# Kernel optimization log

Measured on AMD Instinct MI355X. Metric: run time of the kernel, lower is better.

Reference implementation:

```python
import jax, jax.numpy as jnp
import numpy as np

SIZE = 32  # voxel grid resolution (build_image default)
BIG = 1e9


def voxelize(points, vals, mask, size=SIZE):
    """Faithful dense re-expression of build_image's fractional box-overlap
    rasterization. points [P,3], vals [P], mask [P] -> volume [size,size,size].
    Each point is a cube of side grid_step in normalized coords; its value is
    splatted with separable fractional overlap onto the size^3 grid."""
    pm = jnp.where(mask[:, None], points, BIG)
    mins = jnp.min(pm, axis=0)
    maxs = jnp.max(jnp.where(mask[:, None], points, -BIG), axis=0)
    ranges = maxs - mins
    max_range = jnp.max(ranges) + 1.0
    gs = 1.0 / max_range                      # grid_step
    v = (points - mins - ranges / 2 - 0.5) * gs + 0.5   # [P,3] normalized cube mins
    ns = 1.0 / size                           # new_step
    lo = jnp.arange(size, dtype=points.dtype) * ns       # [S] cell lower edges
    # separable overlap fraction per axis: [P,3,S]
    ov = jnp.clip(jnp.minimum(v[:, :, None] + gs, lo + ns)
                  - jnp.maximum(v[:, :, None], lo), 0.0) / gs
    w = vals * mask.astype(vals.dtype)
    return jnp.einsum('p,pi,pj,pk->ijk', w, ov[:, 0], ov[:, 1], ov[:, 2])


def conv_block(x, W, b, stride):
    y = jax.lax.conv_general_dilated(
        x, W, (stride,) * 3, 'SAME',
        dimension_numbers=('NCDHW', 'OIDHW', 'NCDHW'))
    return jax.nn.relu(y + b[None, :, None, None, None])


def encoder(vox, W1, b1, W2, b2, W3, b3, Wfc, bfc):
    x = vox[:, None]                          # [E,1,32,32,32]
    x = conv_block(x, W1, b1, 2)              # [E,16,16,16,16]
    x = conv_block(x, W2, b2, 2)              # [E,32,8,8,8]
    x = conv_block(x, W3, b3, 2)              # [E,64,4,4,4]
    pooled = x.mean(axis=(2, 3, 4))           # [E,64]
    return pooled @ Wfc + bfc


def setup_inputs() -> dict:
    key = jax.random.key(0)
    ks = jax.random.split(key, 10)
    N, C, P, E = 32768, 256, 128, 1024
    data = jax.random.normal(ks[0], (N, 5), dtype=jnp.float32)
    clusts = jax.random.randint(ks[1], (C, P), 0, N, dtype=jnp.int32)
    clust_mask = jnp.ones((C, P), dtype=bool)
    edge_index = jax.random.randint(ks[2], (2, E), 0, C, dtype=jnp.int64)
    s = 0.1
    W1 = jax.random.normal(ks[3], (16, 1, 3, 3, 3), jnp.float32) * s
    b1 = jnp.zeros((16,), jnp.float32)
    W2 = jax.random.normal(ks[4], (32, 16, 3, 3, 3), jnp.float32) * s
    b2 = jnp.zeros((32,), jnp.float32)
    W3 = jax.random.normal(ks[5], (64, 32, 3, 3, 3), jnp.float32) * s
    b3 = jnp.zeros((64,), jnp.float32)
    Wfc = jax.random.normal(ks[6], (64, 64), jnp.float32) * s
    bfc = jnp.zeros((64,), jnp.float32)
    return {"data": data, "clusts": clusts, "clust_mask": clust_mask,
            "edge_index": edge_index, "W1": W1, "b1": b1, "W2": W2, "b2": b2,
            "W3": W3, "b3": b3, "Wfc": Wfc, "bfc": bfc}


def reference(data, clusts, clust_mask, edge_index, W1, b1, W2, b2, W3, b3, Wfc, bfc):
    # original detaches data before voxelization (numpy round-trip)
    d = jax.lax.stop_gradient(data)

    def edge_vox(cid):
        idx = clusts[cid]                     # [P]
        pts = d[idx, :3]
        vals = d[idx, 4]
        return voxelize(pts, vals, clust_mask[cid])

    ei, ej = edge_index[0], edge_index[1]
    # both clusters of an edge share the same sparse batch id i -> duplicate
    # coordinates sum, i.e. the two independently-normalized images add up
    vox = jax.vmap(edge_vox)(ei) + jax.vmap(edge_vox)(ej)   # [E,32,32,32]
    return encoder(vox, W1, b1, W2, b2, W3, b3, Wfc, bfc)   # [E,64]
```

## Files before the change

kernel.cpp:

```cpp
#include <hip/hip_runtime.h>

#define PPC 128

__device__ __forceinline__ float ovlap(float v, float gs, float inv_gs, int i) {
  const float ns = 0.03125f;
  float lo = (float)i * ns;
  float o  = fminf(v + gs, lo + ns) - fmaxf(v, lo);
  return fmaxf(o, 0.0f) * inv_gs;
}

__global__ __launch_bounds__(256) void k_vox_conv1(
    const float* __restrict__ data,
    const int*   __restrict__ clusts,
    const unsigned char* __restrict__ maskb,
    const float* __restrict__ W1,
    float* __restrict__ y1)
{
  __shared__ float vox[32768];
  __shared__ float rmn[PPC * 3];
  __shared__ float rmx[PPC * 3];
  const int c = blockIdx.x;
  const int t = threadIdx.x;

  for (int i = t; i < 32768; i += 256) vox[i] = 0.f;

  const bool m32 = (maskb[1] == 0);

  if (t < PPC) {
    int idx = clusts[c * PPC + t];
    const float* dp = data + idx * 5;
    bool m = m32 ? (((const int*)maskb)[c * PPC + t] != 0)
                 : (maskb[c * PPC + t] != 0);
#pragma unroll
    for (int d = 0; d < 3; ++d) {
      float p = dp[d];
      rmn[t * 3 + d] = m ? p : 1e9f;
      rmx[t * 3 + d] = m ? p : -1e9f;
    }
  }
  __syncthreads();
  for (int off = 64; off >= 1; off >>= 1) {
    if (t < off) {
#pragma unroll
      for (int d = 0; d < 3; ++d) {
        rmn[t * 3 + d] = fminf(rmn[t * 3 + d], rmn[(t + off) * 3 + d]);
        rmx[t * 3 + d] = fmaxf(rmx[t * 3 + d], rmx[(t + off) * 3 + d]);
      }
    }
    __syncthreads();
  }
  const float mn0 = rmn[0], mn1 = rmn[1], mn2 = rmn[2];
  const float rg0 = rmx[0] - mn0, rg1 = rmx[1] - mn1, rg2 = rmx[2] - mn2;
  const float mr = fmaxf(rg0, fmaxf(rg1, rg2)) + 1.0f;
  const float gs = 1.0f / mr;
  const float inv_gs = 1.0f / gs;

  {
    const int p = t >> 1, h = t & 1;
    int idx = clusts[c * PPC + p];
    const float* dp = data + idx * 5;
    bool m = m32 ? (((const int*)maskb)[c * PPC + p] != 0)
                 : (maskb[c * PPC + p] != 0);
    float w = m ? dp[4] : 0.f;
    if (w != 0.f) {
      float v0 = (dp[0] - mn0 - rg0 * 0.5f - 0.5f) * gs + 0.5f;
      float v1 = (dp[1] - mn1 - rg1 * 0.5f - 0.5f) * gs + 0.5f;
      float v2 = (dp[2] - mn2 - rg2 * 0.5f - 0.5f) * gs + 0.5f;
      int i0 = max(0, (int)floorf(v0 * 32.f) - 1), i1 = min(31, (int)floorf((v0 + gs) * 32.f) + 1);
      int j0 = max(0, (int)floorf(v1 * 32.f) - 1), j1 = min(31, (int)floorf((v1 + gs) * 32.f) + 1);
      int k0 = max(0, (int)floorf(v2 * 32.f) - 1), k1 = min(31, (int)floorf((v2 + gs) * 32.f) + 1);
      for (int i = i0 + h; i <= i1; i += 2) {
        float oi = ovlap(v0, gs, inv_gs, i);
        if (oi <= 0.f) continue;
        float wi = w * oi;
        for (int j = j0; j <= j1; ++j) {
          float oj = ovlap(v1, gs, inv_gs, j);
          if (oj <= 0.f) continue;
          float wij = wi * oj;
          for (int k = k0; k <= k1; ++k) {
            float ok = ovlap(v2, gs, inv_gs, k);
            if (ok > 0.f) atomicAdd(&vox[(i << 10) + (j << 5) + k], wij * ok);
          }
        }
      }
    }
  }
  __syncthreads();

  for (int si = 0; si < 16; ++si) {
    int s = t + (si << 8);
    int oz = s >> 8, oy = (s >> 4) & 15, ox = s & 15;
    float xv[27];
#pragma unroll
    for (int td = 0; td < 3; ++td)
#pragma unroll
      for (int th = 0; th < 3; ++th)
#pragma unroll
        for (int tw = 0; tw < 3; ++tw) {
          int z = 2 * oz + td, y = 2 * oy + th, x = 2 * ox + tw;
          bool okb = (z < 32) & (y < 32) & (x < 32);
          xv[(td * 3 + th) * 3 + tw] = okb ? vox[(z << 10) + (y << 5) + x] : 0.f;
        }
#pragma unroll
    for (int oc = 0; oc < 16; ++oc) {
      float a = 0.f;
#pragma unroll
      for (int tp = 0; tp < 27; ++tp) a = fmaf(W1[oc * 27 + tp], xv[tp], a);
      y1[(((c << 4) + oc) << 12) + s] = a;
    }
  }
}

#define S1 4913
__global__ __launch_bounds__(256) void k_edge(
    const void*  __restrict__ eidx_raw,
    const float* __restrict__ y1,
    const float* __restrict__ b1,
    const float* __restrict__ W2,
    const float* __restrict__ b2,
    const float* __restrict__ W3,
    const float* __restrict__ b3,
    const float* __restrict__ Wfc,
    const float* __restrict__ bfc,
    float* __restrict__ out,
    int E)
{
  __shared__ float smem[2 * S1 + 64];
  float* pooled = smem + 2 * S1;
  const int e = blockIdx.x;
  const int t = threadIdx.x;

  const int* e32 = (const int*)eidx_raw;
  const long long* e64 = (const long long*)eidx_raw;
  const bool is64 = (e32[1] == 0) & (e32[3] == 0) & (e32[5] == 0) & (e32[7] == 0);
  const int ca = is64 ? (int)e64[e] : e32[e];
  const int cb = is64 ? (int)e64[E + e] : e32[E + e];
  const float* Ap = y1 + (size_t)ca * 65536;
  const float* Bp = y1 + (size_t)cb * 65536;

  float acc2[2][32];
#pragma unroll
  for (int h = 0; h < 2; ++h)
#pragma unroll
    for (int o = 0; o < 32; ++o) acc2[h][o] = 0.f;

  const int oz0 = t >> 6, oy0 = (t >> 3) & 7, ox0 = t & 7;
  const int xl = t & 15;
  const int stw = (t >> 4) * 17 + (xl >> 1) + (xl & 1) * 9;

  for (int i = t; i < 2 * S1; i += 256) smem[i] = 0.f;

  {
    const float bb = b1[0];
#pragma unroll 4
    for (int z = 0; z < 16; ++z)
      smem[stw + z * 289] = fmaxf(Ap[(z << 8) + t] + Bp[(z << 8) + t] + bb, 0.f);
  }
  __syncthreads();

#pragma unroll 2
  for (int ic = 0; ic < 16; ++ic) {
    if (ic < 15) {
      const int icn = ic + 1;
      const float* Aic = Ap + (icn << 12);
      const float* Bic = Bp + (icn << 12);
      const float bb = b1[icn];
      const int wb = (icn & 1) * S1 + stw;
#pragma unroll 4
      for (int z = 0; z < 16; ++z)
        smem[wb + z * 289] = fmaxf(Aic[(z << 8) + t] + Bic[(z << 8) + t] + bb, 0.f);
    }
    {
      const int rb = (ic & 1) * S1 + oz0 * 578 + oy0 * 34;
      float xv0[27], xv1[27];
#pragma unroll
      for (int td = 0; td < 3; ++td)
#pragma unroll
        for (int th = 0; th < 3; ++th) {
          const int b0 = rb + td * 289 + th * 17;
          const int tpb = (td * 3 + th) * 3;
          xv0[tpb + 0] = smem[b0 + ox0];
          xv0[tpb + 1] = smem[b0 + 9 + ox0];
          xv0[tpb + 2] = smem[b0 + ox0 + 1];
          xv1[tpb + 0] = smem[b0 + 2312 + ox0];
          xv1[tpb + 1] = smem[b0 + 2312 + 9 + ox0];
          xv1[tpb + 2] = smem[b0 + 2312 + ox0 + 1];
        }
      const float* wrow = W2 + ic * 27;
#pragma unroll
      for (int oc = 0; oc < 32; ++oc) {
#pragma unroll
        for (int tp = 0; tp < 27; ++tp) {
          const float w = wrow[oc * 432 + tp];
          acc2[0][oc] = fmaf(w, xv0[tp], acc2[0][oc]);
          acc2[1][oc] = fmaf(w, xv1[tp], acc2[1][oc]);
        }
      }
    }
    __syncthreads();
  }

  float acc3[16];
#pragma unroll
  for (int o = 0; o < 16; ++o) acc3[o] = 0.f;
  const int l = t & 63, wid = t >> 6;
  const int OZ = l >> 4, OY = (l >> 2) & 3, OX = l & 3;
  const int rb3 = OZ * 162 + OY * 18;
  const int cox = (ox0 >> 1) + (ox0 & 1) * 5;

#pragma unroll
  for (int q = 0; q < 4; ++q) {
    for (int i = t; i < 5832; i += 256) smem[i] = 0.f;
    __syncthreads();
#pragma unroll
    for (int h = 0; h < 2; ++h)
#pragma unroll
      for (int o = 0; o < 8; ++o) {
        const int oc = (q << 3) + o;
        smem[o * 729 + (oz0 + (h << 2)) * 81 + oy0 * 9 + cox] =
            fmaxf(acc2[h][oc] + b2[oc], 0.f);
      }
    __syncthreads();
#pragma unroll 1
    for (int icl = 0; icl < 8; ++icl) {
      const int ic3 = (q << 3) + icl;
      float xv[27];
#pragma unroll
      for (int td = 0; td < 3; ++td)
#pragma unroll
        for (int th = 0; th < 3; ++th) {
          const int bb = icl * 729 + rb3 + td * 81 + th * 9;
          const int tpb = (td * 3 + th) * 3;
          xv[tpb + 0] = smem[bb + OX];
          xv[tpb + 1] = smem[bb + 5 + OX];
          xv[tpb + 2] = smem[bb + OX + 1];
        }
#pragma unroll
      for (int o = 0; o < 16; ++o) {
        const int oc = (wid << 4) + o;
        const float* wr = W3 + (oc * 32 + ic3) * 27;
#pragma unroll
        for (int tp = 0; tp < 27; ++tp) acc3[o] = fmaf(wr[tp], xv[tp], acc3[o]);
      }
    }
    __syncthreads();
  }

#pragma unroll
  for (int o = 0; o < 16; ++o) {
    float r = fmaxf(acc3[o] + b3[(wid << 4) + o], 0.f);
    r += __shfl_xor(r, 1);
    r += __shfl_xor(r, 2);
    r += __shfl_xor(r, 4);
    r += __shfl_xor(r, 8);
    r += __shfl_xor(r, 16);
    r += __shfl_xor(r, 32);
    if (l == 0) pooled[(wid << 4) + o] = r * 0.015625f;
  }
  __syncthreads();
  if (t < 64) {
    float a = bfc[t];
#pragma unroll 8
    for (int k = 0; k < 64; ++k) a = fmaf(pooled[k], Wfc[(k << 6) + t], a);
    out[e * 64 + t] = a;
  }
}

extern "C" void kernel_launch(void* const* d_in, const int* in_sizes, int n_in,
                              void* d_out, int out_size, void* d_ws, size_t ws_size,
                              hipStream_t stream) {
  const float* data = (const float*)d_in[0];
  const int*   clusts = (const int*)d_in[1];
  const unsigned char* maskb = (const unsigned char*)d_in[2];
  const void*  eidx = d_in[3];
  const float* W1 = (const float*)d_in[4];
  const float* b1 = (const float*)d_in[5];
  const float* W2 = (const float*)d_in[6];
  const float* b2 = (const float*)d_in[7];
  const float* W3 = (const float*)d_in[8];
  const float* b3 = (const float*)d_in[9];
  const float* Wfc = (const float*)d_in[10];
  const float* bfc = (const float*)d_in[11];

  const int C = in_sizes[1] / PPC;
  const int E = in_sizes[3] / 2;

  float* y1 = (float*)d_ws;

  k_vox_conv1<<<C, 256, 0, stream>>>(data, clusts, maskb, W1, y1);
  k_edge<<<E, 256, 0, stream>>>(eidx, y1, b1, W2, b2, W3, b3, Wfc, bfc,
                                (float*)d_out, E);
}
```

Baseline: 930.4 us.

## Vectorize staging loads and interleave prefetch with conv2/conv3 tap loops

Staging of the conv1 output (A+B+bias, relu) into shared memory now uses float4 global loads with a remapped store pattern. The loads for the next input channel are split into two halves and issued between groups of the conv2 tap loop, so global latency overlaps with FMAs. The conv2 and conv3 inner loops are restructured to load three taps at a time instead of holding 27-element register arrays, which is meant to reduce register pressure. The conv3 shared buffer is zeroed once rather than per quarter, relying on the halo staying zero across quarters. The risks are the extra synchronisation added at the start and possible changes to scheduling and register allocation.

```diff
diff --git a/kernel.cpp b/kernel.cpp
--- a/kernel.cpp
+++ b/kernel.cpp
@@ -145,60 +145,116 @@
     for (int o = 0; o < 32; ++o) acc2[h][o] = 0.f;
 
   const int oz0 = t >> 6, oy0 = (t >> 3) & 7, ox0 = t & 7;
-  const int xl = t & 15;
-  const int stw = (t >> 4) * 17 + (xl >> 1) + (xl & 1) * 9;
+  const int zl = t >> 6, lane63 = t & 63, xq = t & 3;
+  const int stwb = ((t >> 2) & 15) * 17 + 2 * xq;
 
   for (int i = t; i < 2 * S1; i += 256) smem[i] = 0.f;
+  __syncthreads();
 
   {
+    const float4* A4 = (const float4*)Ap;
+    const float4* B4 = (const float4*)Bp;
     const float bb = b1[0];
-#pragma unroll 4
-    for (int z = 0; z < 16; ++z)
-      smem[stw + z * 289] = fmaxf(Ap[(z << 8) + t] + Bp[(z << 8) + t] + bb, 0.f);
+#pragma unroll
+    for (int b = 0; b < 4; ++b) {
+      const int z = (b << 2) + zl;
+      float4 av = A4[(z << 6) + lane63];
+      float4 bv = B4[(z << 6) + lane63];
+      const int w = z * 289 + stwb;
+      smem[w]      = fmaxf(av.x + bv.x + bb, 0.f);
+      smem[w + 9]  = fmaxf(av.y + bv.y + bb, 0.f);
+      smem[w + 1]  = fmaxf(av.z + bv.z + bb, 0.f);
+      smem[w + 10] = fmaxf(av.w + bv.w + bb, 0.f);
+    }
   }
   __syncthreads();
 
 #pragma unroll 2
   for (int ic = 0; ic < 16; ++ic) {
-    if (ic < 15) {
-      const int icn = ic + 1;
-      const float* Aic = Ap + (icn << 12);
-      const float* Bic = Bp + (icn << 12);
-      const float bb = b1[icn];
-      const int wb = (icn & 1) * S1 + stw;
-#pragma unroll 4
-      for (int z = 0; z < 16; ++z)
-        smem[wb + z * 289] = fmaxf(Aic[(z << 8) + t] + Bic[(z << 8) + t] + bb, 0.f);
-    }
-    {
-      const int rb = (ic & 1) * S1 + oz0 * 578 + oy0 * 34;
-      float xv0[27], xv1[27];
-#pragma unroll
-      for (int td = 0; td < 3; ++td)
-#pragma unroll
-        for (int th = 0; th < 3; ++th) {
-          const int b0 = rb + td * 289 + th * 17;
-          const int tpb = (td * 3 + th) * 3;
-          xv0[tpb + 0] = smem[b0 + ox0];
-          xv0[tpb + 1] = smem[b0 + 9 + ox0];
-          xv0[tpb + 2] = smem[b0 + ox0 + 1];
-          xv1[tpb + 0] = smem[b0 + 2312 + ox0];
-          xv1[tpb + 1] = smem[b0 + 2312 + 9 + ox0];
-          xv1[tpb + 2] = smem[b0 + 2312 + ox0 + 1];
-        }
-      const float* wrow = W2 + ic * 27;
+    const int rb = (ic & 1) * S1 + oz0 * 578 + oy0 * 34;
+    const float* wrow = W2 + ic * 27;
+    const bool st = (ic < 15);
+    const float4* An4 = (const float4*)(Ap + ((ic + 1) << 12));
+    const float4* Bn4 = (const float4*)(Bp + ((ic + 1) << 12));
+    const float bb = st ? b1[ic + 1] : 0.f;
+    const int wb = ((ic + 1) & 1) * S1;
+
+    float4 a0, a1, c0, c1;
+    if (st) {
+      a0 = An4[(zl << 6) + lane63];        c0 = Bn4[(zl << 6) + lane63];
+      a1 = An4[((4 + zl) << 6) + lane63];  c1 = Bn4[((4 + zl) << 6) + lane63];
+    }
+#pragma unroll
+    for (int g = 0; g < 4; ++g) {
+      const int td = g / 3, th = g % 3;
+      const int b0 = rb + td * 289 + th * 17;
+      float t00 = smem[b0 + ox0], t01 = smem[b0 + 9 + ox0], t02 = smem[b0 + ox0 + 1];
+      float t10 = smem[b0 + 2312 + ox0], t11 = smem[b0 + 2312 + 9 + ox0], t12 = smem[b0 + 2312 + ox0 + 1];
+      const int tp = g * 3;
 #pragma unroll
       for (int oc = 0; oc < 32; ++oc) {
-#pragma unroll
-        for (int tp = 0; tp < 27; ++tp) {
-          const float w = wrow[oc * 432 + tp];
-          acc2[0][oc] = fmaf(w, xv0[tp], acc2[0][oc]);
-          acc2[1][oc] = fmaf(w, xv1[tp], acc2[1][oc]);
-        }
-      }
+        const float w0 = wrow[oc * 432 + tp];
+        const float w1 = wrow[oc * 432 + tp + 1];
+        const float w2 = wrow[oc * 432 + tp + 2];
+        acc2[0][oc] = fmaf(w0, t00, acc2[0][oc]);
+        acc2[0][oc] = fmaf(w1, t01, acc2[0][oc]);
+        acc2[0][oc] = fmaf(w2, t02, acc2[0][oc]);
+        acc2[1][oc] = fmaf(w0, t10, acc2[1][oc]);
+        acc2[1][oc] = fmaf(w1, t11, acc2[1][oc]);
+        acc2[1][oc] = fmaf(w2, t12, acc2[1][oc]);
+      }
+    }
+    if (st) {
+      const int w0 = wb + zl * 289 + stwb;
+      smem[w0]      = fmaxf(a0.x + c0.x + bb, 0.f);
+      smem[w0 + 9]  = fmaxf(a0.y + c0.y + bb, 0.f);
+      smem[w0 + 1]  = fmaxf(a0.z + c0.z + bb, 0.f);
+      smem[w0 + 10] = fmaxf(a0.w + c0.w + bb, 0.f);
+      const int w1 = wb + (4 + zl) * 289 + stwb;
+      smem[w1]      = fmaxf(a1.x + c1.x + bb, 0.f);
+      smem[w1 + 9]  = fmaxf(a1.y + c1.y + bb, 0.f);
+      smem[w1 + 1]  = fmaxf(a1.z + c1.z + bb, 0.f);
+      smem[w1 + 10] = fmaxf(a1.w + c1.w + bb, 0.f);
+      a0 = An4[((8 + zl) << 6) + lane63];   c0 = Bn4[((8 + zl) << 6) + lane63];
+      a1 = An4[((12 + zl) << 6) + lane63];  c1 = Bn4[((12 + zl) << 6) + lane63];
+    }
+#pragma unroll
+    for (int g = 4; g < 9; ++g) {
+      const int td = g / 3, th = g % 3;
+      const int b0 = rb + td * 289 + th * 17;
+      float t00 = smem[b0 + ox0], t01 = smem[b0 + 9 + ox0], t02 = smem[b0 + ox0 + 1];
+      float t10 = smem[b0 + 2312 + ox0], t11 = smem[b0 + 2312 + 9 + ox0], t12 = smem[b0 + 2312 + ox0 + 1];
+      const int tp = g * 3;
+#pragma unroll
+      for (int oc = 0; oc < 32; ++oc) {
+        const float w0 = wrow[oc * 432 + tp];
+        const float w1 = wrow[oc * 432 + tp + 1];
+        const float w2 = wrow[oc * 432 + tp + 2];
+        acc2[0][oc] = fmaf(w0, t00, acc2[0][oc]);
+        acc2[0][oc] = fmaf(w1, t01, acc2[0][oc]);
+        acc2[0][oc] = fmaf(w2, t02, acc2[0][oc]);
+        acc2[1][oc] = fmaf(w0, t10, acc2[1][oc]);
+        acc2[1][oc] = fmaf(w1, t11, acc2[1][oc]);
+        acc2[1][oc] = fmaf(w2, t12, acc2[1][oc]);
+      }
+    }
+    if (st) {
+      const int w0 = wb + (8 + zl) * 289 + stwb;
+      smem[w0]      = fmaxf(a0.x + c0.x + bb, 0.f);
+      smem[w0 + 9]  = fmaxf(a0.y + c0.y + bb, 0.f);
+      smem[w0 + 1]  = fmaxf(a0.z + c0.z + bb, 0.f);
+      smem[w0 + 10] = fmaxf(a0.w + c0.w + bb, 0.f);
+      const int w1 = wb + (12 + zl) * 289 + stwb;
+      smem[w1]      = fmaxf(a1.x + c1.x + bb, 0.f);
+      smem[w1 + 9]  = fmaxf(a1.y + c1.y + bb, 0.f);
+      smem[w1 + 1]  = fmaxf(a1.z + c1.z + bb, 0.f);
+      smem[w1 + 10] = fmaxf(a1.w + c1.w + bb, 0.f);
     }
     __syncthreads();
   }
+
+  for (int i = t; i < 5832; i += 256) smem[i] = 0.f;
+  __syncthreads();
 
   float acc3[16];
 #pragma unroll
@@ -210,8 +266,6 @@
 
 #pragma unroll
   for (int q = 0; q < 4; ++q) {
-    for (int i = t; i < 5832; i += 256) smem[i] = 0.f;
-    __syncthreads();
 #pragma unroll
     for (int h = 0; h < 2; ++h)
 #pragma unroll
@@ -224,23 +278,23 @@
 #pragma unroll 1
     for (int icl = 0; icl < 8; ++icl) {
       const int ic3 = (q << 3) + icl;
-      float xv[27];
-#pragma unroll
-      for (int td = 0; td < 3; ++td)
-#pragma unroll
-        for (int th = 0; th < 3; ++th) {
-          const int bb = icl * 729 + rb3 + td * 81 + th * 9;
-          const int tpb = (td * 3 + th) * 3;
-          xv[tpb + 0] = smem[bb + OX];
-          xv[tpb + 1] = smem[bb + 5 + OX];
-          xv[tpb + 2] = smem[bb + OX + 1];
+      const int bbse = icl * 729 + rb3;
+      const float* wr3 = W3 + ic3 * 27;
+#pragma unroll
+      for (int g = 0; g < 9; ++g) {
+        const int td = g / 3, th = g % 3;
+        const int ba = bbse + td * 81 + th * 9;
+        float u0 = smem[ba + OX];
+        float u1 = smem[ba + 5 + OX];
+        float u2 = smem[ba + OX + 1];
+        const int tp = g * 3;
+#pragma unroll
+        for (int o = 0; o < 16; ++o) {
+          const float* wr = wr3 + ((wid << 4) + o) * 864;
+          acc3[o] = fmaf(wr[tp],     u0, acc3[o]);
+          acc3[o] = fmaf(wr[tp + 1], u1, acc3[o]);
+          acc3[o] = fmaf(wr[tp + 2], u2, acc3[o]);
         }
-#pragma unroll
-      for (int o = 0; o < 16; ++o) {
-        const int oc = (wid << 4) + o;
-        const float* wr = W3 + (oc * 32 + ic3) * 27;
-#pragma unroll
-        for (int tp = 0; tp < 27; ++tp) acc3[o] = fmaf(wr[tp], xv[tp], acc3[o]);
       }
     }
     __syncthreads();
```

Result: slower. 1.972 ms (+111.9%).

## Double k_edge block size, one conv2 output per thread, float4 y1 loads

Applied to the files above, without the earlier changes.

The edge kernel now runs 512 threads per block instead of 256. Each thread computes one conv2 output position for all 32 channels rather than two, and conv3 work is split across 8 waves of 8 output channels each. The y1 tiles are read as float4 and scattered into the strided shared-memory layout. Next-channel loads are issued before the conv2 math so global latency overlaps compute. The aim is lower register pressure per thread and more resident waves, at the cost of reloading weights across twice as many threads.

```diff
diff --git a/kernel.cpp b/kernel.cpp
--- a/kernel.cpp
+++ b/kernel.cpp
@@ -112,7 +112,7 @@
 }
 
 #define S1 4913
-__global__ __launch_bounds__(256) void k_edge(
+__global__ __launch_bounds__(512) void k_edge(
     const void*  __restrict__ eidx_raw,
     const float* __restrict__ y1,
     const float* __restrict__ b1,
@@ -138,71 +138,92 @@
   const float* Ap = y1 + (size_t)ca * 65536;
   const float* Bp = y1 + (size_t)cb * 65536;
 
-  float acc2[2][32];
-#pragma unroll
-  for (int h = 0; h < 2; ++h)
-#pragma unroll
-    for (int o = 0; o < 32; ++o) acc2[h][o] = 0.f;
+  float acc2[32];
+#pragma unroll
+  for (int o = 0; o < 32; ++o) acc2[o] = 0.f;
 
   const int oz0 = t >> 6, oy0 = (t >> 3) & 7, ox0 = t & 7;
-  const int xl = t & 15;
-  const int stw = (t >> 4) * 17 + (xl >> 1) + (xl & 1) * 9;
-
-  for (int i = t; i < 2 * S1; i += 256) smem[i] = 0.f;
+  const int stw = ((t >> 2) & 15) * 17 + 2 * (t & 3);
+  const int sz0 = t >> 6;
+
+  for (int i = t; i < 2 * S1; i += 512) smem[i] = 0.f;
+  __syncthreads();
 
   {
+    const float4* A4 = (const float4*)Ap;
+    const float4* B4 = (const float4*)Bp;
     const float bb = b1[0];
-#pragma unroll 4
-    for (int z = 0; z < 16; ++z)
-      smem[stw + z * 289] = fmaxf(Ap[(z << 8) + t] + Bp[(z << 8) + t] + bb, 0.f);
-  }
-  __syncthreads();
-
-#pragma unroll 2
+    float4 av0 = A4[t],      bv0 = B4[t];
+    float4 av1 = A4[512 + t], bv1 = B4[512 + t];
+    const int w0 = sz0 * 289 + stw;
+    smem[w0]      = fmaxf(av0.x + bv0.x + bb, 0.f);
+    smem[w0 + 9]  = fmaxf(av0.y + bv0.y + bb, 0.f);
+    smem[w0 + 1]  = fmaxf(av0.z + bv0.z + bb, 0.f);
+    smem[w0 + 10] = fmaxf(av0.w + bv0.w + bb, 0.f);
+    const int w1 = (8 + sz0) * 289 + stw;
+    smem[w1]      = fmaxf(av1.x + bv1.x + bb, 0.f);
+    smem[w1 + 9]  = fmaxf(av1.y + bv1.y + bb, 0.f);
+    smem[w1 + 1]  = fmaxf(av1.z + bv1.z + bb, 0.f);
+    smem[w1 + 10] = fmaxf(av1.w + bv1.w + bb, 0.f);
+  }
+  __syncthreads();
+
+#pragma unroll 1
   for (int ic = 0; ic < 16; ++ic) {
-    if (ic < 15) {
-      const int icn = ic + 1;
-      const float* Aic = Ap + (icn << 12);
-      const float* Bic = Bp + (icn << 12);
-      const float bb = b1[icn];
-      const int wb = (icn & 1) * S1 + stw;
-#pragma unroll 4
-      for (int z = 0; z < 16; ++z)
-        smem[wb + z * 289] = fmaxf(Aic[(z << 8) + t] + Bic[(z << 8) + t] + bb, 0.f);
-    }
-    {
-      const int rb = (ic & 1) * S1 + oz0 * 578 + oy0 * 34;
-      float xv0[27], xv1[27];
-#pragma unroll
-      for (int td = 0; td < 3; ++td)
-#pragma unroll
-        for (int th = 0; th < 3; ++th) {
-          const int b0 = rb + td * 289 + th * 17;
-          const int tpb = (td * 3 + th) * 3;
-          xv0[tpb + 0] = smem[b0 + ox0];
-          xv0[tpb + 1] = smem[b0 + 9 + ox0];
-          xv0[tpb + 2] = smem[b0 + ox0 + 1];
-          xv1[tpb + 0] = smem[b0 + 2312 + ox0];
-          xv1[tpb + 1] = smem[b0 + 2312 + 9 + ox0];
-          xv1[tpb + 2] = smem[b0 + 2312 + ox0 + 1];
+    const int rb = (ic & 1) * S1 + oz0 * 578 + oy0 * 34;
+    const float* wrow = W2 + ic * 27;
+    const bool st = (ic < 15);
+    float4 a0, a1, c0, c1;
+    if (st) {
+      const float4* An4 = (const float4*)(Ap + ((ic + 1) << 12));
+      const float4* Bn4 = (const float4*)(Bp + ((ic + 1) << 12));
+      a0 = An4[t];        c0 = Bn4[t];
+      a1 = An4[512 + t];  c1 = Bn4[512 + t];
+    }
+#pragma unroll
+    for (int td = 0; td < 3; ++td) {
+      float xv[9];
+#pragma unroll
+      for (int th = 0; th < 3; ++th) {
+        const int b0 = rb + td * 289 + th * 17;
+        xv[th * 3 + 0] = smem[b0 + ox0];
+        xv[th * 3 + 1] = smem[b0 + 9 + ox0];
+        xv[th * 3 + 2] = smem[b0 + ox0 + 1];
+      }
+#pragma unroll
+      for (int ocp = 0; ocp < 16; ++ocp) {
+        const float* wa = wrow + (2 * ocp) * 432 + td * 9;
+        const float* wc = wrow + (2 * ocp + 1) * 432 + td * 9;
+#pragma unroll
+        for (int j = 0; j < 9; ++j) {
+          acc2[2 * ocp]     = fmaf(wa[j], xv[j], acc2[2 * ocp]);
+          acc2[2 * ocp + 1] = fmaf(wc[j], xv[j], acc2[2 * ocp + 1]);
         }
-      const float* wrow = W2 + ic * 27;
-#pragma unroll
-      for (int oc = 0; oc < 32; ++oc) {
-#pragma unroll
-        for (int tp = 0; tp < 27; ++tp) {
-          const float w = wrow[oc * 432 + tp];
-          acc2[0][oc] = fmaf(w, xv0[tp], acc2[0][oc]);
-          acc2[1][oc] = fmaf(w, xv1[tp], acc2[1][oc]);
-        }
-      }
+      }
+    }
+    if (st) {
+      const float bb = b1[ic + 1];
+      const int wbuf = ((ic + 1) & 1) * S1;
+      const int w0 = wbuf + sz0 * 289 + stw;
+      smem[w0]      = fmaxf(a0.x + c0.x + bb, 0.f);
+      smem[w0 + 9]  = fmaxf(a0.y + c0.y + bb, 0.f);
+      smem[w0 + 1]  = fmaxf(a0.z + c0.z + bb, 0.f);
+      smem[w0 + 10] = fmaxf(a0.w + c0.w + bb, 0.f);
+      const int w1 = wbuf + (8 + sz0) * 289 + stw;
+      smem[w1]      = fmaxf(a1.x + c1.x + bb, 0.f);
+      smem[w1 + 9]  = fmaxf(a1.y + c1.y + bb, 0.f);
+      smem[w1 + 1]  = fmaxf(a1.z + c1.z + bb, 0.f);
+      smem[w1 + 10] = fmaxf(a1.w + c1.w + bb, 0.f);
     }
     __syncthreads();
   }
 
-  float acc3[16];
-#pragma unroll
-  for (int o = 0; o < 16; ++o) acc3[o] = 0.f;
+  for (int i = t; i < 5832; i += 512) smem[i] = 0.f;
+  __syncthreads();
+
+  float acc3[8];
+#pragma unroll
+  for (int o = 0; o < 8; ++o) acc3[o] = 0.f;
   const int l = t & 63, wid = t >> 6;
   const int OZ = l >> 4, OY = (l >> 2) & 3, OX = l & 3;
   const int rb3 = OZ * 162 + OY * 18;
@@ -210,52 +231,45 @@
 
 #pragma unroll
   for (int q = 0; q < 4; ++q) {
-    for (int i = t; i < 5832; i += 256) smem[i] = 0.f;
-    __syncthreads();
-#pragma unroll
-    for (int h = 0; h < 2; ++h)
-#pragma unroll
-      for (int o = 0; o < 8; ++o) {
-        const int oc = (q << 3) + o;
-        smem[o * 729 + (oz0 + (h << 2)) * 81 + oy0 * 9 + cox] =
-            fmaxf(acc2[h][oc] + b2[oc], 0.f);
-      }
+#pragma unroll
+    for (int o = 0; o < 8; ++o) {
+      const int oc = (q << 3) + o;
+      smem[o * 729 + oz0 * 81 + oy0 * 9 + cox] = fmaxf(acc2[oc] + b2[oc], 0.f);
+    }
     __syncthreads();
 #pragma unroll 1
     for (int icl = 0; icl < 8; ++icl) {
       const int ic3 = (q << 3) + icl;
-      float xv[27];
-#pragma unroll
-      for (int td = 0; td < 3; ++td)
-#pragma unroll
-        for (int th = 0; th < 3; ++th) {
-          const int bb = icl * 729 + rb3 + td * 81 + th * 9;
-          const int tpb = (td * 3 + th) * 3;
-          xv[tpb + 0] = smem[bb + OX];
-          xv[tpb + 1] = smem[bb + 5 + OX];
-          xv[tpb + 2] = smem[bb + OX + 1];
+      const int bbse = icl * 729 + rb3;
+#pragma unroll
+      for (int g = 0; g < 9; ++g) {
+        const int ba = bbse + (g / 3) * 81 + (g % 3) * 9;
+        const float u0 = smem[ba + OX];
+        const float u1 = smem[ba + 5 + OX];
+        const float u2 = smem[ba + OX + 1];
+        const int tp = g * 3;
+#pragma unroll
+        for (int o = 0; o < 8; ++o) {
+          const float* wr = W3 + (((wid << 3) + o) * 32 + ic3) * 27;
+          acc3[o] = fmaf(wr[tp],     u0, acc3[o]);
+          acc3[o] = fmaf(wr[tp + 1], u1, acc3[o]);
+          acc3[o] = fmaf(wr[tp + 2], u2, acc3[o]);
         }
-#pragma unroll
-      for (int o = 0; o < 16; ++o) {
-        const int oc = (wid << 4) + o;
-        const float* wr = W3 + (oc * 32 + ic3) * 27;
-#pragma unroll
-        for (int tp = 0; tp < 27; ++tp) acc3[o] = fmaf(wr[tp], xv[tp], acc3[o]);
       }
     }
     __syncthreads();
   }
 
 #pragma unroll
-  for (int o = 0; o < 16; ++o) {
-    float r = fmaxf(acc3[o] + b3[(wid << 4) + o], 0.f);
+  for (int o = 0; o < 8; ++o) {
+    float r = fmaxf(acc3[o] + b3[(wid << 3) + o], 0.f);
     r += __shfl_xor(r, 1);
     r += __shfl_xor(r, 2);
     r += __shfl_xor(r, 4);
     r += __shfl_xor(r, 8);
     r += __shfl_xor(r, 16);
     r += __shfl_xor(r, 32);
-    if (l == 0) pooled[(wid << 4) + o] = r * 0.015625f;
+    if (l == 0) pooled[(wid << 3) + o] = r * 0.015625f;
   }
   __syncthreads();
   if (t < 64) {
@@ -288,6 +302,6 @@
   float* y1 = (float*)d_ws;
 
   k_vox_conv1<<<C, 256, 0, stream>>>(data, clusts, maskb, W1, y1);
-  k_edge<<<E, 256, 0, stream>>>(eidx, y1, b1, W2, b2, W3, b3, Wfc, bfc,
+  k_edge<<<E, 512, 0, stream>>>(eidx, y1, b1, W2, b2, W3, b3, Wfc, bfc,
                                 (float*)d_out, E);
 }
```

After: 1.804 ms. +93.9%, slower.

## Vectorize conv2 input staging with float4 and batch two channels per sync

Applied to the files above, without the earlier changes.

Layer-1 activations are now read with float4 loads and scattered into the padded, parity-split shared tile, two input channels per group. The old per-channel double-buffered prefetch, which overlapped the next channel's load with the current channel's compute, is replaced by load-then-compute phases with one barrier pair per two channels. The zeroing of the conv3 staging buffer is hoisted out of the q loop, because only interior cells are rewritten each pass and the halo stays zero. The intent is fewer global load instructions and fewer barriers, at the cost of losing load/compute overlap inside the block.

```diff
diff --git a/kernel.cpp b/kernel.cpp
--- a/kernel.cpp
+++ b/kernel.cpp
@@ -145,33 +145,36 @@
     for (int o = 0; o < 32; ++o) acc2[h][o] = 0.f;
 
   const int oz0 = t >> 6, oy0 = (t >> 3) & 7, ox0 = t & 7;
-  const int xl = t & 15;
-  const int stw = (t >> 4) * 17 + (xl >> 1) + (xl & 1) * 9;
+  const int sty = ((t >> 2) & 15) * 17 + 2 * (t & 3);
+  const int stz = t >> 6;
 
   for (int i = t; i < 2 * S1; i += 256) smem[i] = 0.f;
 
-  {
-    const float bb = b1[0];
-#pragma unroll 4
-    for (int z = 0; z < 16; ++z)
-      smem[stw + z * 289] = fmaxf(Ap[(z << 8) + t] + Bp[(z << 8) + t] + bb, 0.f);
-  }
-  __syncthreads();
-
+  for (int icg = 0; icg < 8; ++icg) {
+    __syncthreads();
+#pragma unroll
+    for (int icl = 0; icl < 2; ++icl) {
+      const int ic = icg * 2 + icl;
+      const float4* A4 = (const float4*)(Ap + (ic << 12));
+      const float4* B4 = (const float4*)(Bp + (ic << 12));
+      const float bb = b1[ic];
+      const int wb = icl * S1;
 #pragma unroll 2
-  for (int ic = 0; ic < 16; ++ic) {
-    if (ic < 15) {
-      const int icn = ic + 1;
-      const float* Aic = Ap + (icn << 12);
-      const float* Bic = Bp + (icn << 12);
-      const float bb = b1[icn];
-      const int wb = (icn & 1) * S1 + stw;
-#pragma unroll 4
-      for (int z = 0; z < 16; ++z)
-        smem[wb + z * 289] = fmaxf(Aic[(z << 8) + t] + Bic[(z << 8) + t] + bb, 0.f);
-    }
-    {
-      const int rb = (ic & 1) * S1 + oz0 * 578 + oy0 * 34;
+      for (int p = 0; p < 4; ++p) {
+        float4 av = A4[p * 256 + t];
+        float4 bv = B4[p * 256 + t];
+        const int w = wb + ((p << 2) + stz) * 289 + sty;
+        smem[w]      = fmaxf(av.x + bv.x + bb, 0.f);
+        smem[w + 9]  = fmaxf(av.y + bv.y + bb, 0.f);
+        smem[w + 1]  = fmaxf(av.z + bv.z + bb, 0.f);
+        smem[w + 10] = fmaxf(av.w + bv.w + bb, 0.f);
+      }
+    }
+    __syncthreads();
+#pragma unroll 1
+    for (int icl = 0; icl < 2; ++icl) {
+      const int ic = icg * 2 + icl;
+      const int rb = icl * S1 + oz0 * 578 + oy0 * 34;
       float xv0[27], xv1[27];
 #pragma unroll
       for (int td = 0; td < 3; ++td)
@@ -197,8 +200,11 @@
         }
       }
     }
-    __syncthreads();
-  }
+  }
+  __syncthreads();
+
+  for (int i = t; i < 5832; i += 256) smem[i] = 0.f;
+  __syncthreads();
 
   float acc3[16];
 #pragma unroll
@@ -210,8 +216,6 @@
 
 #pragma unroll
   for (int q = 0; q < 4; ++q) {
-    for (int i = t; i < 5832; i += 256) smem[i] = 0.f;
-    __syncthreads();
 #pragma unroll
     for (int h = 0; h < 2; ++h)
 #pragma unroll
```

Result: slower. 1.058 ms (+13.8%).
